# Kernel tuning notes

Measured on AMD Instinct MI355X. Metric: run time of the kernel, lower is better.

Reference implementation:

```python
import jax, jax.numpy as jnp
import numpy as np

B, S1, S2, D1, D2, F = 8, 2048, 2048, 512, 512, 256

def setup_inputs() -> dict:
    key = jax.random.key(0)
    ks = jax.random.split(key, 10)
    sc1 = 1.0 / np.sqrt(D1)
    sc2 = 1.0 / np.sqrt(D2)
    scf = 1.0 / np.sqrt(F)
    return {
        "feat1": jax.random.normal(ks[0], (B, S1, D1), jnp.float32),
        "feat2": jax.random.normal(ks[1], (B, S2, D2), jnp.float32),
        "Wq": jax.random.normal(ks[2], (D1, F), jnp.float32) * sc1,
        "bq": jnp.zeros((F,), jnp.float32),
        "Wk": jax.random.normal(ks[3], (D2, F), jnp.float32) * sc2,
        "bk": jnp.zeros((F,), jnp.float32),
        "Wv": jax.random.normal(ks[4], (D2, F), jnp.float32) * sc2,
        "bv": jnp.zeros((F,), jnp.float32),
        "Wfc": jax.random.normal(ks[5], (F, F), jnp.float32) * scf,
        "bfc": jnp.zeros((F,), jnp.float32),
    }

def reference(feat1, feat2, Wq, bq, Wk, bk, Wv, bv, Wfc, bfc):
    Q = jnp.einsum('bsd,df->bsf', feat1, Wq) + bq          # [B,S1,F]
    K = jnp.einsum('btd,df->btf', feat2, Wk) + bk          # [B,S2,F]
    V = jnp.einsum('btd,df->btf', feat2, Wv) + bv          # [B,S2,F]
    scores = jnp.einsum('bsf,btf->bst', Q, K) / jnp.sqrt(jnp.float32(K.shape[-1]))
    attn = jax.nn.softmax(scores, axis=-1)                 # [B,S1,S2]
    attn_out = jnp.einsum('bst,btf->bsf', attn, V)         # [B,S1,F]
    out = jnp.einsum('bsf,fg->bsg', attn_out, Wfc) + bfc   # [B,S1,F]
    return out
```

## Files before the change

kernel.cpp:

```cpp
#include <hip/hip_runtime.h>
#include <hip/hip_bf16.h>

#define B_ 8
#define S1_ 2048
#define S2_ 2048
#define D_ 512
#define F_ 256

typedef __attribute__((ext_vector_type(4))) float f32x4;
typedef __attribute__((ext_vector_type(8))) short s16x8;
typedef __attribute__((ext_vector_type(4))) short s16x4;

__device__ __forceinline__ short f2bf(float x) {
  union { float f; unsigned u; } v; v.f = x;
  unsigned r = v.u + 0x7fffu + ((v.u >> 16) & 1u);
  return (short)(r >> 16);
}

__device__ __forceinline__ int pk2bf(float a, float b) {
  union { __hip_bfloat162 h; int i; } u;
  u.h = __float22bfloat162_rn(make_float2(a, b));
  return u.i;
}

__global__ __launch_bounds__(256) void wtrans_kernel(
    const float* __restrict__ Wq, const float* __restrict__ Wk,
    const float* __restrict__ Wv, const float* __restrict__ Wfc,
    short* __restrict__ Wqt, short* __restrict__ Wkt,
    short* __restrict__ Wvt, short* __restrict__ Wfct) {
  int y = blockIdx.y;
  const float* W; short* Wt; int D;
  if (y == 0)      { W = Wq;  Wt = Wqt;  D = 512; }
  else if (y == 1) { W = Wk;  Wt = Wkt;  D = 512; }
  else if (y == 2) { W = Wv;  Wt = Wvt;  D = 512; }
  else             { W = Wfc; Wt = Wfct; D = 256; }
  int tiles_d = D >> 6;
  int bx = blockIdx.x;
  if (bx >= tiles_d * 4) return;
  int d0 = (bx % tiles_d) * 64, f0 = (bx / tiles_d) * 64;

  __shared__ short Ts[64][68];
  int t = threadIdx.x;
  int r = t >> 2, c16 = (t & 3) * 16;
  {
    const float* src = W + (size_t)(d0 + r) * F_ + f0 + c16;
    f32x4 v0 = *(const f32x4*)(src);
    f32x4 v1 = *(const f32x4*)(src + 4);
    f32x4 v2 = *(const f32x4*)(src + 8);
    f32x4 v3 = *(const f32x4*)(src + 12);
    s16x8 s0, s1;
    ((int*)&s0)[0] = pk2bf(v0[0], v0[1]); ((int*)&s0)[1] = pk2bf(v0[2], v0[3]);
    ((int*)&s0)[2] = pk2bf(v1[0], v1[1]); ((int*)&s0)[3] = pk2bf(v1[2], v1[3]);
    ((int*)&s1)[0] = pk2bf(v2[0], v2[1]); ((int*)&s1)[1] = pk2bf(v2[2], v2[3]);
    ((int*)&s1)[2] = pk2bf(v3[0], v3[1]); ((int*)&s1)[3] = pk2bf(v3[2], v3[3]);
    *(s16x8*)(&Ts[r][c16]) = s0;
    *(s16x8*)(&Ts[r][c16 + 8]) = s1;
  }
  __syncthreads();
  {
    int fr = t >> 2, dc16 = (t & 3) * 16;
    s16x8 o0, o1;
    for (int j = 0; j < 8; ++j) o0[j] = Ts[dc16 + j][fr];
    for (int j = 0; j < 8; ++j) o1[j] = Ts[dc16 + 8 + j][fr];
    short* dst = Wt + (size_t)(f0 + fr) * D + d0 + dc16;
    *(s16x8*)dst = o0;
    *(s16x8*)(dst + 8) = o1;
  }
}

__global__ __launch_bounds__(256, 3) void proj_kernel(
    const float* __restrict__ feat1, const float* __restrict__ feat2,
    const short* __restrict__ Wqt, const short* __restrict__ Wkt,
    const short* __restrict__ Wvt,
    const float* __restrict__ bq, const float* __restrict__ bk,
    const float* __restrict__ bv,
    short* __restrict__ Qw, short* __restrict__ Kw, short* __restrict__ Vtw) {
  const float* A; const short* Wt; const float* bias; short* outp;
  float scale; int trans;
  if (blockIdx.y == 0)      { A = feat1; Wt = Wqt; bias = bq; outp = Qw;  scale = 0.0625f; trans = 0; }
  else if (blockIdx.y == 1) { A = feat2; Wt = Wkt; bias = bk; outp = Kw;  scale = 1.0f;    trans = 0; }
  else                      { A = feat2; Wt = Wvt; bias = bv; outp = Vtw; scale = 1.0f;    trans = 1; }

  __shared__ __align__(16) short As[64][72];
  __shared__ __align__(16) short Ws[256][72];

  int m0 = blockIdx.x * 64;
  int t = threadIdx.x;
  int w = t >> 6, L = t & 63, rowA = L & 15, quad = L >> 4;
  int ar = t >> 2, ac16 = (t & 3) * 16;

  f32x4 acc[4][4];
  for (int i = 0; i < 4; ++i)
    for (int j = 0; j < 4; ++j) acc[i][j] = (f32x4){0.f, 0.f, 0.f, 0.f};

  for (int k0 = 0; k0 < D_; k0 += 64) {
    {
      const float* src = A + (size_t)(m0 + ar) * D_ + k0 + ac16;
      f32x4 v0 = *(const f32x4*)(src);
      f32x4 v1 = *(const f32x4*)(src + 4);
      f32x4 v2 = *(const f32x4*)(src + 8);
      f32x4 v3 = *(const f32x4*)(src + 12);
      s16x8 s0, s1;
      ((int*)&s0)[0] = pk2bf(v0[0], v0[1]); ((int*)&s0)[1] = pk2bf(v0[2], v0[3]);
      ((int*)&s0)[2] = pk2bf(v1[0], v1[1]); ((int*)&s0)[3] = pk2bf(v1[2], v1[3]);
      ((int*)&s1)[0] = pk2bf(v2[0], v2[1]); ((int*)&s1)[1] = pk2bf(v2[2], v2[3]);
      ((int*)&s1)[2] = pk2bf(v3[0], v3[1]); ((int*)&s1)[3] = pk2bf(v3[2], v3[3]);
      *(s16x8*)(&As[ar][ac16]) = s0;
      *(s16x8*)(&As[ar][ac16 + 8]) = s1;
    }
    for (int p = 0; p < 4; ++p) {
      int r = (t >> 2) + p * 64;
      const short* src = Wt + (size_t)r * D_ + k0 + ac16;
      *(s16x8*)(&Ws[r][ac16]) = *(const s16x8*)(src);
      *(s16x8*)(&Ws[r][ac16 + 8]) = *(const s16x8*)(src + 8);
    }
    __syncthreads();
    for (int kt = 0; kt < 2; ++kt) {
      s16x8 a[4];
      for (int mt = 0; mt < 4; ++mt)
        a[mt] = *(const s16x8*)(&As[mt * 16 + rowA][kt * 32 + quad * 8]);
      for (int nt = 0; nt < 4; ++nt) {
        s16x8 bfr = *(const s16x8*)(&Ws[w * 64 + nt * 16 + rowA][kt * 32 + quad * 8]);
        for (int mt = 0; mt < 4; ++mt)
          acc[mt][nt] = __builtin_amdgcn_mfma_f32_16x16x32_bf16(a[mt], bfr, acc[mt][nt], 0, 0, 0);
      }
    }
    __syncthreads();
  }

  if (!trans) {
    float bn[4];
    for (int nt = 0; nt < 4; ++nt) bn[nt] = bias[w * 64 + nt * 16 + rowA];
    for (int mt = 0; mt < 4; ++mt) {
      int m = m0 + mt * 16 + quad * 4;
      for (int nt = 0; nt < 4; ++nt) {
        int n = w * 64 + nt * 16 + rowA;
        for (int r = 0; r < 4; ++r)
          outp[(size_t)(m + r) * F_ + n] = f2bf((acc[mt][nt][r] + bn[nt]) * scale);
      }
    }
  } else {
    int bb = m0 >> 11;
    int tbase = m0 & (S2_ - 1);
    float bn[4];
    for (int nt = 0; nt < 4; ++nt) bn[nt] = bias[w * 64 + nt * 16 + rowA];
    for (int nt = 0; nt < 4; ++nt) {
      int f = w * 64 + nt * 16 + rowA;
      for (int mt = 0; mt < 4; ++mt) {
        int tt = tbase + mt * 16 + quad * 4;
        s16x4 o;
        for (int r = 0; r < 4; ++r) o[r] = f2bf(acc[mt][nt][r] + bn[nt]);
        *(s16x4*)(outp + ((size_t)bb * F_ + f) * S2_ + tt) = o;
      }
    }
  }
}

__global__ __launch_bounds__(512, 2) void flash_kernel(
    const short* __restrict__ Q,
    const short* __restrict__ K,
    const short* __restrict__ Vt,
    short* __restrict__ O) {
  __shared__ __align__(16) short Ks[2][64][264];
  __shared__ __align__(16) short Vs[2][256][72];
  __shared__ __align__(16) short Ps[2][64][72];

  int b = blockIdx.x & 7;
  int s0 = (blockIdx.x >> 3) * 64;
  int t = threadIdx.x;
  int w = t >> 6, L = t & 63, rowA = L & 15, quad = L >> 4;
  int isS = (w < 4);

  const short* Kb = K + (size_t)b * S2_ * F_;
  const short* Vb = Vt + (size_t)b * F_ * S2_;

  int kr = t >> 5, kc8 = (t & 31) * 8;
  int vr = t >> 3, vc8 = (t & 7) * 8;

  int rs = (w & 1) * 32, cs = ((w >> 1) & 1) * 32;
  int mg = (w - 4) & 1, fg = ((w - 4) >> 1) & 1;

  s16x8 qf[2][8];
  if (isS) {
    const short* Qb = Q + ((size_t)b * S1_ + s0 + rs) * F_;
    for (int mt = 0; mt < 2; ++mt)
      for (int kt = 0; kt < 8; ++kt)
        qf[mt][kt] = *(const s16x8*)(Qb + (size_t)(mt * 16 + rowA) * F_ + kt * 32 + quad * 8);
  }
  f32x4 o[2][8];
  for (int i = 0; i < 2; ++i)
    for (int j = 0; j < 8; ++j) o[i][j] = (f32x4){0.f, 0.f, 0.f, 0.f};
  float l_lane[2][4] = {{0.f,0.f,0.f,0.f},{0.f,0.f,0.f,0.f}};

  s16x8 kpre[4], vpre[4];
  for (int p = 0; p < 4; ++p)
    kpre[p] = *(const s16x8*)(Kb + (size_t)(kr + p * 16) * F_ + kc8);
  for (int p = 0; p < 4; ++p)
    *(s16x8*)(&Ks[0][kr + p * 16][kc8]) = kpre[p];
  for (int p = 0; p < 4; ++p)
    kpre[p] = *(const s16x8*)(Kb + (size_t)(64 + kr + p * 16) * F_ + kc8);
  for (int p = 0; p < 4; ++p)
    vpre[p] = *(const s16x8*)(Vb + (size_t)(vr + p * 64) * S2_ + vc8);

  for (int it = 0; it <= 32; ++it) {
    int cb = it & 1;
    __syncthreads();
    if (it < 32) {
      for (int p = 0; p < 4; ++p)
        *(s16x8*)(&Vs[cb][vr + p * 64][vc8]) = vpre[p];
      if (it < 31) {
        for (int p = 0; p < 4; ++p)
          *(s16x8*)(&Ks[1 - cb][kr + p * 16][kc8]) = kpre[p];
        int n0 = (it + 1) * 64;
        for (int p = 0; p < 4; ++p)
          vpre[p] = *(const s16x8*)(Vb + (size_t)(vr + p * 64) * S2_ + n0 + vc8);
      }
      if (it < 30) {
        int n0 = (it + 2) * 64;
        for (int p = 0; p < 4; ++p)
          kpre[p] = *(const s16x8*)(Kb + (size_t)(n0 + kr + p * 16) * F_ + kc8);
      }
    }
    if (isS) {
      if (it < 32) {
        f32x4 s[2][2];
        for (int i = 0; i < 2; ++i)
          for (int j = 0; j < 2; ++j) s[i][j] = (f32x4){0.f, 0.f, 0.f, 0.f};
        for (int kt = 0; kt < 8; ++kt) {
          s16x8 bf0 = *(const s16x8*)(&Ks[cb][cs + rowA][kt * 32 + quad * 8]);
          s16x8 bf1 = *(const s16x8*)(&Ks[cb][cs + 16 + rowA][kt * 32 + quad * 8]);
          for (int mt = 0; mt < 2; ++mt) {
            s[mt][0] = __builtin_amdgcn_mfma_f32_16x16x32_bf16(qf[mt][kt], bf0, s[mt][0], 0, 0, 0);
            s[mt][1] = __builtin_amdgcn_mfma_f32_16x16x32_bf16(qf[mt][kt], bf1, s[mt][1], 0, 0, 0);
          }
        }
        for (int mt = 0; mt < 2; ++mt)
          for (int nt = 0; nt < 2; ++nt)
            for (int r = 0; r < 4; ++r) {
              float p = __expf(s[mt][nt][r]);
              l_lane[mt][r] += p;
              Ps[cb][rs + mt * 16 + quad * 4 + r][cs + nt * 16 + rowA] = f2bf(p);
            }
      }
    } else {
      if (it > 0) {
        int pb = 1 - cb;
        s16x8 pa[2][2];
        for (int mt = 0; mt < 2; ++mt)
          for (int kt = 0; kt < 2; ++kt)
            pa[mt][kt] = *(const s16x8*)(&Ps[pb][mg * 32 + mt * 16 + rowA][kt * 32 + quad * 8]);
        for (int ft = 0; ft < 8; ++ft)
          for (int kt = 0; kt < 2; ++kt) {
            s16x8 vf = *(const s16x8*)(&Vs[pb][fg * 128 + ft * 16 + rowA][kt * 32 + quad * 8]);
            for (int mt = 0; mt < 2; ++mt)
              o[mt][ft] = __builtin_amdgcn_mfma_f32_16x16x32_bf16(pa[mt][kt], vf, o[mt][ft], 0, 0, 0);
          }
      }
    }
  }

  float* lf = (float*)&Ks[0][0][0];
  if (isS) {
    for (int mt = 0; mt < 2; ++mt)
      for (int r = 0; r < 4; ++r) {
        float x = l_lane[mt][r];
        for (int off = 1; off < 16; off <<= 1)
          x += __shfl_xor(x, off, 64);
        if (rowA == 0)
          lf[((w >> 1) & 1) * 64 + rs + mt * 16 + quad * 4 + r] = x;
      }
  }
  __syncthreads();
  if (!isS) {
    short* Ob = O + ((size_t)b * S1_ + s0) * F_;
    for (int mt = 0; mt < 2; ++mt)
      for (int r = 0; r < 4; ++r) {
        int row = mg * 32 + mt * 16 + quad * 4 + r;
        float inv = 1.0f / (lf[row] + lf[64 + row]);
        for (int ft = 0; ft < 8; ++ft)
          Ob[(size_t)row * F_ + fg * 128 + ft * 16 + rowA] = f2bf(o[mt][ft][r] * inv);
      }
  }
}

__global__ __launch_bounds__(256) void fc_kernel(
    const short* __restrict__ AO,
    const short* __restrict__ Wt,
    const float* __restrict__ bias,
    float* __restrict__ out) {
  __shared__ __align__(16) short As[64][72];
  __shared__ __align__(16) short Ws[128][72];

  int m0 = blockIdx.x * 64;
  int n0 = blockIdx.y * 128;
  int t = threadIdx.x;
  int w = t >> 6, L = t & 63, rowA = L & 15, quad = L >> 4;
  int wy = w & 1, wx = w >> 1;

  int ar = t >> 2, ac16 = (t & 3) * 16;
  int wr = t >> 1, wc32 = (t & 1) * 32;

  s16x8 apre[2], wpre[4];
  {
    const short* asrc = AO + (size_t)(m0 + ar) * F_ + ac16;
    apre[0] = *(const s16x8*)(asrc);
    apre[1] = *(const s16x8*)(asrc + 8);
    const short* wsrc = Wt + (size_t)(n0 + wr) * F_ + wc32;
    for (int j = 0; j < 4; ++j) wpre[j] = *(const s16x8*)(wsrc + j * 8);
  }

  f32x4 acc[2][4];
  for (int i = 0; i < 2; ++i)
    for (int j = 0; j < 4; ++j) acc[i][j] = (f32x4){0.f, 0.f, 0.f, 0.f};

  for (int k0 = 0; k0 < F_; k0 += 64) {
    *(s16x8*)(&As[ar][ac16]) = apre[0];
    *(s16x8*)(&As[ar][ac16 + 8]) = apre[1];
    for (int j = 0; j < 4; ++j) *(s16x8*)(&Ws[wr][wc32 + j * 8]) = wpre[j];
    __syncthreads();
    if (k0 + 64 < F_) {
      const short* asrc = AO + (size_t)(m0 + ar) * F_ + k0 + 64 + ac16;
      apre[0] = *(const s16x8*)(asrc);
      apre[1] = *(const s16x8*)(asrc + 8);
      const short* wsrc = Wt + (size_t)(n0 + wr) * F_ + k0 + 64 + wc32;
      for (int j = 0; j < 4; ++j) wpre[j] = *(const s16x8*)(wsrc + j * 8);
    }
    for (int kt = 0; kt < 2; ++kt) {
      s16x8 a[2];
      for (int mt = 0; mt < 2; ++mt)
        a[mt] = *(const s16x8*)(&As[wy * 32 + mt * 16 + rowA][kt * 32 + quad * 8]);
      for (int nt = 0; nt < 4; ++nt) {
        s16x8 bfr = *(const s16x8*)(&Ws[wx * 64 + nt * 16 + rowA][kt * 32 + quad * 8]);
        for (int mt = 0; mt < 2; ++mt)
          acc[mt][nt] = __builtin_amdgcn_mfma_f32_16x16x32_bf16(a[mt], bfr, acc[mt][nt], 0, 0, 0);
      }
    }
    __syncthreads();
  }

  float bn[4];
  for (int nt = 0; nt < 4; ++nt) bn[nt] = bias[n0 + wx * 64 + nt * 16 + rowA];
  for (int mt = 0; mt < 2; ++mt) {
    int m = m0 + wy * 32 + mt * 16 + quad * 4;
    for (int nt = 0; nt < 4; ++nt) {
      int n = n0 + wx * 64 + nt * 16 + rowA;
      for (int r = 0; r < 4; ++r)
        out[(size_t)(m + r) * F_ + n] = acc[mt][nt][r] + bn[nt];
    }
  }
}

extern "C" void kernel_launch(void* const* d_in, const int* in_sizes, int n_in,
                              void* d_out, int out_size, void* d_ws, size_t ws_size,
                              hipStream_t stream) {
  const float* feat1 = (const float*)d_in[0];
  const float* feat2 = (const float*)d_in[1];
  const float* Wq  = (const float*)d_in[2];
  const float* bq  = (const float*)d_in[3];
  const float* Wk  = (const float*)d_in[4];
  const float* bk  = (const float*)d_in[5];
  const float* Wv  = (const float*)d_in[6];
  const float* bv  = (const float*)d_in[7];
  const float* Wfc = (const float*)d_in[8];
  const float* bfc = (const float*)d_in[9];
  float* out = (float*)d_out;
  char* ws = (char*)d_ws;

  short* Qw   = (short*)(ws);
  short* Kw   = (short*)(ws + (size_t)(8u  << 20));
  short* Vtw  = (short*)(ws + (size_t)(16u << 20));
  short* AOw  = (short*)(ws + (size_t)(24u << 20));
  short* Wqt  = (short*)(ws + (size_t)(32u << 20));
  short* Wkt  = Wqt + 256 * 512;
  short* Wvt  = Wkt + 256 * 512;
  short* Wfct = Wvt + 256 * 512;

  wtrans_kernel<<<dim3(32, 4), 256, 0, stream>>>(Wq, Wk, Wv, Wfc, Wqt, Wkt, Wvt, Wfct);
  proj_kernel<<<dim3(256, 3), 256, 0, stream>>>(feat1, feat2, Wqt, Wkt, Wvt,
                                                bq, bk, bv, Qw, Kw, Vtw);
  flash_kernel<<<dim3(256), 512, 0, stream>>>(Qw, Kw, Vtw, AOw);
  fc_kernel<<<dim3(256, 2), 256, 0, stream>>>(AOw, Wfct, bfc, out);
}
```

Measured before the change: 190.7 us.

## Add dedicated loader warps to flash kernel for warp-specialized K/V staging

Grows the flash block from 512 to 1024 threads. The 8 new wavefronts only load K and V tiles from global memory into shared memory, while the score and PV wavefronts no longer issue global loads. The register prefetch depth drops: each loader wave fetches and stores within the same iteration. This removes load work and prefetch registers from the compute waves, but raises per-block register and thread pressure and may expose global latency because loads are no longer prefetched ahead.

```diff
diff --git a/kernel.cpp b/kernel.cpp
--- a/kernel.cpp
+++ b/kernel.cpp
@@ -156,7 +156,7 @@
   }
 }
 
-__global__ __launch_bounds__(512, 2) void flash_kernel(
+__global__ __launch_bounds__(1024) void flash_kernel(
     const short* __restrict__ Q,
     const short* __restrict__ K,
     const short* __restrict__ Vt,
@@ -169,16 +169,17 @@
   int s0 = (blockIdx.x >> 3) * 64;
   int t = threadIdx.x;
   int w = t >> 6, L = t & 63, rowA = L & 15, quad = L >> 4;
-  int isS = (w < 4);
+  int isS = (w < 4), isPV = (w >= 4 && w < 8);
 
   const short* Kb = K + (size_t)b * S2_ * F_;
   const short* Vb = Vt + (size_t)b * F_ * S2_;
 
-  int kr = t >> 5, kc8 = (t & 31) * 8;
-  int vr = t >> 3, vc8 = (t & 7) * 8;
-
   int rs = (w & 1) * 32, cs = ((w >> 1) & 1) * 32;
   int mg = (w - 4) & 1, fg = ((w - 4) >> 1) & 1;
+
+  int u = t - 512;
+  int kr = u >> 5, kc8 = (u & 31) * 8;
+  int vr = u >> 3, vc8 = (u & 7) * 8;
 
   s16x8 qf[2][8];
   if (isS) {
@@ -192,36 +193,34 @@
     for (int j = 0; j < 8; ++j) o[i][j] = (f32x4){0.f, 0.f, 0.f, 0.f};
   float l_lane[2][4] = {{0.f,0.f,0.f,0.f},{0.f,0.f,0.f,0.f}};
 
-  s16x8 kpre[4], vpre[4];
-  for (int p = 0; p < 4; ++p)
-    kpre[p] = *(const s16x8*)(Kb + (size_t)(kr + p * 16) * F_ + kc8);
-  for (int p = 0; p < 4; ++p)
-    *(s16x8*)(&Ks[0][kr + p * 16][kc8]) = kpre[p];
-  for (int p = 0; p < 4; ++p)
-    kpre[p] = *(const s16x8*)(Kb + (size_t)(64 + kr + p * 16) * F_ + kc8);
-  for (int p = 0; p < 4; ++p)
-    vpre[p] = *(const s16x8*)(Vb + (size_t)(vr + p * 64) * S2_ + vc8);
+  if (w >= 8) {
+    for (int p = 0; p < 4; ++p) {
+      s16x8 kv = *(const s16x8*)(Kb + (size_t)(kr + p * 16) * F_ + kc8);
+      *(s16x8*)(&Ks[0][kr + p * 16][kc8]) = kv;
+    }
+  }
 
   for (int it = 0; it <= 32; ++it) {
     int cb = it & 1;
     __syncthreads();
-    if (it < 32) {
-      for (int p = 0; p < 4; ++p)
-        *(s16x8*)(&Vs[cb][vr + p * 64][vc8]) = vpre[p];
-      if (it < 31) {
+    if (w >= 8) {
+      if (it < 32) {
+        int n0 = it * 64;
+        s16x8 vv[4];
         for (int p = 0; p < 4; ++p)
-          *(s16x8*)(&Ks[1 - cb][kr + p * 16][kc8]) = kpre[p];
-        int n0 = (it + 1) * 64;
+          vv[p] = *(const s16x8*)(Vb + (size_t)(vr + p * 64) * S2_ + n0 + vc8);
         for (int p = 0; p < 4; ++p)
-          vpre[p] = *(const s16x8*)(Vb + (size_t)(vr + p * 64) * S2_ + n0 + vc8);
-      }
-      if (it < 30) {
-        int n0 = (it + 2) * 64;
-        for (int p = 0; p < 4; ++p)
-          kpre[p] = *(const s16x8*)(Kb + (size_t)(n0 + kr + p * 16) * F_ + kc8);
-      }
-    }
-    if (isS) {
+          *(s16x8*)(&Vs[cb][vr + p * 64][vc8]) = vv[p];
+        if (it < 31) {
+          int n1 = (it + 1) * 64;
+          s16x8 kv[4];
+          for (int p = 0; p < 4; ++p)
+            kv[p] = *(const s16x8*)(Kb + (size_t)(n1 + kr + p * 16) * F_ + kc8);
+          for (int p = 0; p < 4; ++p)
+            *(s16x8*)(&Ks[1 - cb][kr + p * 16][kc8]) = kv[p];
+        }
+      }
+    } else if (isS) {
       if (it < 32) {
         f32x4 s[2][2];
         for (int i = 0; i < 2; ++i)
@@ -271,7 +270,7 @@
       }
   }
   __syncthreads();
-  if (!isS) {
+  if (isPV) {
     short* Ob = O + ((size_t)b * S1_ + s0) * F_;
     for (int mt = 0; mt < 2; ++mt)
       for (int r = 0; r < 4; ++r) {
@@ -378,6 +377,6 @@
   wtrans_kernel<<<dim3(32, 4), 256, 0, stream>>>(Wq, Wk, Wv, Wfc, Wqt, Wkt, Wvt, Wfct);
   proj_kernel<<<dim3(256, 3), 256, 0, stream>>>(feat1, feat2, Wqt, Wkt, Wvt,
                                                 bq, bk, bv, Qw, Kw, Vtw);
-  flash_kernel<<<dim3(256), 512, 0, stream>>>(Qw, Kw, Vtw, AOw);
+  flash_kernel<<<dim3(256), 1024, 0, stream>>>(Qw, Kw, Vtw, AOw);
   fc_kernel<<<dim3(256, 2), 256, 0, stream>>>(AOw, Wfct, bfc, out);
 }
```

Measured after the change: 246.1 us. +29.0%, slower.
